# Kernel optimization log

Measured on AMD Instinct MI355X. Metric: run time of the kernel, lower is better.

Reference implementation:

```python
import jax, jax.numpy as jnp
import numpy as np

EPS_BN = 1e-5
EPS_LN = 1e-5
OUT_H, OUT_W = 256, 256


def conv2d(x, w, b, pad):
    y = jax.lax.conv_general_dilated(x, w, (1, 1), [(pad, pad), (pad, pad)],
                                     dimension_numbers=('NCHW', 'OIHW', 'NCHW'))
    return y + b[None, :, None, None]


def leaky(x):
    return jnp.where(x >= 0, x, 0.2 * x)


def bn_eval(x, g, b):
    # fresh BatchNorm2d in eval mode: running_mean=0, running_var=1
    scale = g / jnp.sqrt(1.0 + EPS_BN)
    return x * scale[None, :, None, None] + b[None, :, None, None]


def resize_bilinear(x, oh, ow):
    # align_corners=True bilinear, separable gathers
    n, c, h, w = x.shape
    sy = jnp.arange(oh, dtype=x.dtype) * ((h - 1) / (oh - 1))
    sx = jnp.arange(ow, dtype=x.dtype) * ((w - 1) / (ow - 1))
    y0 = jnp.clip(jnp.floor(sy).astype(jnp.int32), 0, h - 2)
    x0 = jnp.clip(jnp.floor(sx).astype(jnp.int32), 0, w - 2)
    fy = (sy - y0.astype(x.dtype))[None, None, :, None]
    fx = (sx - x0.astype(x.dtype))[None, None, None, :]
    top = x[:, :, y0, :] * (1 - fy) + x[:, :, y0 + 1, :] * fy        # (n,c,oh,w)
    out = top[:, :, :, x0] * (1 - fx) + top[:, :, :, x0 + 1] * fx    # (n,c,oh,ow)
    return out


def layernorm(x, g, b):
    mu = jnp.mean(x, axis=-1, keepdims=True)
    var = jnp.mean((x - mu) ** 2, axis=-1, keepdims=True)
    return (x - mu) * jax.lax.rsqrt(var + EPS_LN) * g + b


def setup_inputs() -> dict:
    key = jax.random.key(0)
    ks = iter(jax.random.split(key, 64))

    def rn(shape, scale=0.05):
        return (jax.random.normal(next(ks), shape, dtype=jnp.float32) * scale)

    inp = {'x': jax.random.normal(next(ks), (8, 64, 128, 128), dtype=jnp.float32)}
    inp.update(
        r_c7a_w=rn((16, 64, 7, 7)), r_c7a_b=jnp.zeros((16,), jnp.float32),
        r_c1_w=rn((16, 16, 1, 1)), r_c1_b=jnp.zeros((16,), jnp.float32),
        r_bn1_g=1.0 + rn((16,), 0.1), r_bn1_b=jnp.zeros((16,), jnp.float32),
        rb_c1_w=rn((16, 16, 3, 3)), rb_c1_b=jnp.zeros((16,), jnp.float32),
        rb_bn1_g=1.0 + rn((16,), 0.1), rb_bn1_b=jnp.zeros((16,), jnp.float32),
        rb_c2_w=rn((16, 16, 3, 3)), rb_c2_b=jnp.zeros((16,), jnp.float32),
        rb_bn2_g=1.0 + rn((16,), 0.1), rb_bn2_b=jnp.zeros((16,), jnp.float32),
        r_c3_w=rn((16, 16, 3, 3)), r_c3_b=jnp.zeros((16,), jnp.float32),
        r_bn2_g=1.0 + rn((16,), 0.1), r_bn2_b=jnp.zeros((16,), jnp.float32),
        r_c7b_w=rn((64, 16, 7, 7)), r_c7b_b=jnp.zeros((64,), jnp.float32),
        a_k_w=rn((1, 64, 1, 1)), a_k_b=jnp.zeros((1,), jnp.float32),
        a_q_w=rn((1, 64, 1, 1)), a_q_b=jnp.zeros((1,), jnp.float32),
        a_v_w=rn((8, 64, 1, 1)), a_v_b=jnp.zeros((8,), jnp.float32),
        a_r_w=rn((64, 8, 1, 1)), a_r_b=jnp.zeros((64,), jnp.float32),
        t_ln_g=jnp.ones((64,), jnp.float32), t_ln_b=jnp.zeros((64,), jnp.float32),
        t_fc1_w=rn((64, 64)), t_fc1_b=jnp.zeros((64,), jnp.float32),
        t_fc2_w=rn((64, 64)), t_fc2_b=jnp.zeros((64,), jnp.float32),
    )
    return inp


def reference(x, r_c7a_w, r_c7a_b, r_c1_w, r_c1_b, r_bn1_g, r_bn1_b,
              rb_c1_w, rb_c1_b, rb_bn1_g, rb_bn1_b, rb_c2_w, rb_c2_b,
              rb_bn2_g, rb_bn2_b, r_c3_w, r_c3_b, r_bn2_g, r_bn2_b,
              r_c7b_w, r_c7b_b, a_k_w, a_k_b, a_q_w, a_q_b, a_v_w, a_v_b,
              a_r_w, a_r_b, t_ln_g, t_ln_b, t_fc1_w, t_fc1_b, t_fc2_w, t_fc2_b):
    # ---- Resizer ----
    identity = resize_bilinear(x, OUT_H, OUT_W)
    y = leaky(conv2d(x, r_c7a_w, r_c7a_b, 3))
    y = bn_eval(leaky(conv2d(y, r_c1_w, r_c1_b, 0)), r_bn1_g, r_bn1_b)
    y = resize_bilinear(y, OUT_H, OUT_W)
    conv_identity = y
    z = leaky(bn_eval(conv2d(y, rb_c1_w, rb_c1_b, 1), rb_bn1_g, rb_bn1_b))
    z = bn_eval(conv2d(z, rb_c2_w, rb_c2_b, 1), rb_bn2_g, rb_bn2_b) + y
    z = bn_eval(conv2d(z, r_c3_w, r_c3_b, 1), r_bn2_g, r_bn2_b) + conv_identity
    out = conv2d(z, r_c7b_w, r_c7b_b, 3) + identity

    # ---- EfficientAttention (key_channels=1, head_count=1, value_channels=8) ----
    n, c, h, w = out.shape
    hw = h * w
    k = conv2d(out, a_k_w, a_k_b, 0).reshape(n, 1, hw)
    q = conv2d(out, a_q_w, a_q_b, 0).reshape(n, 1, hw)
    v = conv2d(out, a_v_w, a_v_b, 0).reshape(n, 8, hw)
    key = jax.nn.softmax(k, axis=2)            # softmax over spatial positions
    query = jax.nn.softmax(q, axis=1)          # size-1 channel axis -> ones (faithful)
    context = jnp.einsum('nkp,nvp->nkv', key, v)          # (n,1,8)
    att = jnp.einsum('nkv,nkp->nvp', context, query)      # (n,8,hw)
    out = conv2d(att.reshape(n, 8, h, w), a_r_w, a_r_b, 0) + out

    # ---- TransformerBlock (identity conv, 1 encoder: x + MLP(LN(x))) ----
    t = out.reshape(n, c, hw).transpose(2, 0, 1)          # (hw, n, c)
    tn = layernorm(t, t_ln_g, t_ln_b)
    m = jax.nn.gelu(tn @ t_fc1_w.T + t_fc1_b, approximate=False) @ t_fc2_w.T + t_fc2_b
    t = t + m
    return t.transpose(1, 2, 0).reshape(n, c, h, w)
```

## Files before the change

kernel.cpp:

```cpp
#include <hip/hip_runtime.h>
#include <math.h>

#define DI __device__ __forceinline__
#define HW128 (128*128)
#define HW256 (256*256)

__device__ const float BN_RS = 0.9999950000374997f;

DI float leakyf(float x){ return x >= 0.f ? x : 0.2f*x; }

DI unsigned short f2bf(float f){
    unsigned u = __float_as_uint(f);
    return (unsigned short)((u + 0x7fffu + ((u >> 16) & 1u)) >> 16);
}
DI void unpack2(unsigned u, float& lo, float& hi){
    lo = __uint_as_float(u << 16);
    hi = __uint_as_float(u & 0xffff0000u);
}
DI void load8(const uint4* s, size_t idx, unsigned* d){
    uint4 t0 = s[idx], t1 = s[idx + 1];
    d[0]=t0.x; d[1]=t0.y; d[2]=t0.z; d[3]=t0.w;
    d[4]=t1.x; d[5]=t1.y; d[6]=t1.z; d[7]=t1.w;
}

typedef __attribute__((ext_vector_type(8))) short short8v;
typedef __attribute__((ext_vector_type(4))) float float4v;

__global__ __launch_bounds__(256) void prepack(
    const float* __restrict__ w7a, const float* __restrict__ w1,
    const float* __restrict__ w3a, const float* __restrict__ b3a, const float* __restrict__ g3a, const float* __restrict__ be3a,
    const float* __restrict__ w3b, const float* __restrict__ b3b, const float* __restrict__ g3b, const float* __restrict__ be3b,
    const float* __restrict__ w3c, const float* __restrict__ b3c, const float* __restrict__ g3c, const float* __restrict__ be3c,
    const float* __restrict__ w7b, const float* __restrict__ fc1w, const float* __restrict__ fc2w,
    unsigned short* __restrict__ p7aB, float* __restrict__ p1,
    float* __restrict__ q3a, float* __restrict__ q3b, float* __restrict__ q3c,
    unsigned short* __restrict__ w3aB, unsigned short* __restrict__ w3bB, unsigned short* __restrict__ w3cB,
    unsigned short* __restrict__ pwB,
    unsigned short* __restrict__ pwT1, unsigned short* __restrict__ pwT2)
{
    int i = blockIdx.x * 256 + threadIdx.x;
    if (i < 57344) {
        int g = i / 14336, rem = i - g*14336;
        int ks = rem >> 9, oc = (rem >> 5) & 15, k = rem & 31;
        int ky = ks >> 2, kx = ((ks & 3) << 1) + (k >> 4), ic = g*16 + (k & 15);
        p7aB[i] = (kx < 7) ? f2bf(w7a[(oc*64 + ic)*49 + ky*7 + kx]) : (unsigned short)0;
    }
    if (i < 57344) {
        int ks = i >> 11, oc = (i >> 5) & 63, k = i & 31;
        int ky = ks >> 2, kx = ((ks & 3) << 1) + (k >> 4), ic = k & 31 & 15;
        ic = k & 15;
        pwB[i] = (kx < 7) ? f2bf(w7b[((oc*16 + ic)*7 + ky)*7 + kx]) : (unsigned short)0;
    }
    if (i < 3072) {
        int ks = i >> 9, oc = (i >> 5) & 15, k = i & 31;
        int ky = ks >> 1, kx = ((ks & 1) << 1) + (k >> 4), ic = k & 15;
        if (kx < 3) {
            int src = (oc*16 + ic)*9 + ky*3 + kx;
            w3aB[i] = f2bf(w3a[src] * (g3a[oc]*BN_RS));
            w3bB[i] = f2bf(w3b[src] * (g3b[oc]*BN_RS));
            w3cB[i] = f2bf(w3c[src] * (g3c[oc]*BN_RS));
        } else {
            w3aB[i] = 0; w3bB[i] = 0; w3cB[i] = 0;
        }
    }
    if (i < 256) { int oc = i & 15, ic = i >> 4; p1[i] = w1[oc*16 + ic]; }
    if (i < 16) {
        q3a[i] = b3a[i]*(g3a[i]*BN_RS) + be3a[i];
        q3b[i] = b3b[i]*(g3b[i]*BN_RS) + be3b[i];
        q3c[i] = b3c[i]*(g3c[i]*BN_RS) + be3c[i];
    }
    if (i < 4096) { pwT1[i] = f2bf(fc1w[i]); pwT2[i] = f2bf(fc2w[i]); }
}

__global__ __launch_bounds__(256) void x_to_ci(
    const float* __restrict__ x, unsigned short* __restrict__ xci)
{
    int idx = blockIdx.x*256 + threadIdx.x;
    int p = idx & 16383, gn = idx >> 14;
    int g = gn & 3, n = gn >> 2;
    const float* xb = x + (size_t)(n*64 + g*16)*HW128 + p;
    unsigned q[8];
#pragma unroll
    for (int h = 0; h < 8; ++h) {
        float a0 = xb[(size_t)(2*h)*HW128];
        float a1 = xb[(size_t)(2*h + 1)*HW128];
        q[h] = (unsigned)f2bf(a0) | ((unsigned)f2bf(a1) << 16);
    }
    uint4* dst = (uint4*)xci + (size_t)idx*2;
    dst[0] = make_uint4(q[0], q[1], q[2], q[3]);
    dst[1] = make_uint4(q[4], q[5], q[6], q[7]);
}

__global__ __launch_bounds__(256) void conv7a_mfma(
    const unsigned short* __restrict__ xci,
    const unsigned short* __restrict__ pw,
    const float* __restrict__ b7a, const float* __restrict__ p1,
    const float* __restrict__ b1, const float* __restrict__ bng,
    const float* __restrict__ bnb, unsigned short* __restrict__ y2ci)
{
    __shared__ __align__(16) unsigned char lds[17408];
    unsigned short* tile = (unsigned short*)lds;
    float* P16 = (float*)lds;

    const int tid = threadIdx.x;
    const int n = blockIdx.z, ox = blockIdx.x*16, oy = blockIdx.y*16;
    const int w = tid >> 6, l = tid & 63, lg = l >> 4, ln = l & 15;

    float4v acc[4];
#pragma unroll
    for (int mi = 0; mi < 4; ++mi) acc[mi] = (float4v){0.f,0.f,0.f,0.f};

    const uint4* xc4 = (const uint4*)xci;
    uint4* tl4 = (uint4*)tile;
    const short8v* Bb = (const short8v*)pw;

    for (int g = 0; g < 4; ++g) {
        __syncthreads();
        for (int u = tid; u < 1056; u += 256) {
            int r = u / 48, s = u - r*48;
            int y = oy + r - 3, xcol = ox + (s >> 1) - 3;
            uint4 v = make_uint4(0u,0u,0u,0u);
            if (y >= 0 && y < 128 && xcol >= 0 && xcol < 128)
                v = xc4[((size_t)(n*4 + g)*16384 + y*128 + xcol)*2 + (s & 1)];
            tl4[u] = v;
        }
        __syncthreads();
        for (int ks = 0; ks < 28; ++ks) {
            const int ky = ks >> 2, kxp = (ks & 3) << 1;
            short8v b = Bb[(g*28 + ks)*64 + ln*4 + lg];
            short8v a[4];
#pragma unroll
            for (int mi = 0; mi < 4; ++mi) {
                int row = (4*w + mi) + ky;
                a[mi] = *(const short8v*)(tile + (row*24 + ln + kxp)*16 + lg*8);
            }
#pragma unroll
            for (int mi = 0; mi < 4; ++mi)
                acc[mi] = __builtin_amdgcn_mfma_f32_16x16x32_bf16(a[mi], b, acc[mi], 0, 0, 0);
        }
    }
    __syncthreads();
    const float bo = b7a[ln];
#pragma unroll
    for (int mi = 0; mi < 4; ++mi)
#pragma unroll
        for (int r = 0; r < 4; ++r)
            P16[((4*w + mi)*16 + lg*4 + r)*17 + ln] = leakyf(acc[mi][r] + bo);
    __syncthreads();
    const int py = tid >> 4, pxx = tid & 15;
    float lv[16];
#pragma unroll
    for (int ic = 0; ic < 16; ++ic) lv[ic] = P16[tid*17 + ic];
    float u16[16];
#pragma unroll
    for (int o = 0; o < 16; ++o) {
        float u = b1[o];
#pragma unroll
        for (int ic = 0; ic < 16; ++ic) u += lv[ic] * p1[ic*16 + o];
        u = leakyf(u);
        u16[o] = u * (bng[o]*BN_RS) + bnb[o];
    }
    const int p = (oy + py)*128 + ox + pxx;
    unsigned q[8];
#pragma unroll
    for (int h = 0; h < 8; ++h)
        q[h] = (unsigned)f2bf(u16[2*h]) | ((unsigned)f2bf(u16[2*h+1]) << 16);
    uint4* dst = (uint4*)y2ci + (size_t)(n*16384 + p)*2;
    dst[0] = make_uint4(q[0], q[1], q[2], q[3]);
    dst[1] = make_uint4(q[4], q[5], q[6], q[7]);
}

__global__ __launch_bounds__(256) void resize_ci(
    const unsigned short* __restrict__ y2ci, unsigned short* __restrict__ yci)
{
    const int n = blockIdx.z;
    const int ox = blockIdx.x*16 + threadIdx.x;
    const int oy = blockIdx.y*16 + threadIdx.y;
    float sy = oy * (127.f/255.f), sx = ox * (127.f/255.f);
    int y0 = min((int)sy, 126), x0 = min((int)sx, 126);
    float fy = sy - y0, fx = sx - x0;
    const uint4* src = (const uint4*)y2ci;
    size_t i00 = ((size_t)n*16384 + y0*128 + x0)*2;
    unsigned A00[8], A01[8], A10[8], A11[8];
    load8(src, i00,       A00);
    load8(src, i00 + 2,   A01);
    load8(src, i00 + 256, A10);
    load8(src, i00 + 258, A11);
    unsigned q[8];
#pragma unroll
    for (int h = 0; h < 8; ++h) {
        float l00, h00, l01, h01, l10, h10, l11, h11;
        unpack2(A00[h], l00, h00); unpack2(A01[h], l01, h01);
        unpack2(A10[h], l10, h10); unpack2(A11[h], l11, h11);
        float lo = (l00*(1.f-fx) + l01*fx)*(1.f-fy) + (l10*(1.f-fx) + l11*fx)*fy;
        float hi = (h00*(1.f-fx) + h01*fx)*(1.f-fy) + (h10*(1.f-fx) + h11*fx)*fy;
        q[h] = (unsigned)f2bf(lo) | ((unsigned)f2bf(hi) << 16);
    }
    uint4* dst = (uint4*)yci + ((size_t)n*65536 + oy*256 + ox)*2;
    dst[0] = make_uint4(q[0], q[1], q[2], q[3]);
    dst[1] = make_uint4(q[4], q[5], q[6], q[7]);
}

template<int MODE>
__global__ __launch_bounds__(256) void conv3_mfma(
    const unsigned short* __restrict__ in_ci,
    const unsigned short* __restrict__ wB, const float* __restrict__ q3,
    const unsigned short* __restrict__ res_ci,
    unsigned short* __restrict__ out_ci)
{
    __shared__ __align__(16) unsigned char lds[17408];
    unsigned short* tile = (unsigned short*)lds;
    float* P16 = (float*)lds;

    const int tid = threadIdx.x;
    const int n = blockIdx.z, ox = blockIdx.x*16, oy = blockIdx.y*16;
    const int w = tid >> 6, l = tid & 63, lg = l >> 4, ln = l & 15;

    const uint4* zc = (const uint4*)in_ci;
    uint4* tl4 = (uint4*)tile;
    for (int u = tid; u < 720; u += 256) {
        int r = u / 40, s = u - r*40;
        int y = oy + r - 1, xcol = ox + (s >> 1) - 1;
        uint4 v = make_uint4(0u,0u,0u,0u);
        if (y >= 0 && y < 256 && xcol >= 0 && xcol < 256)
            v = zc[((size_t)n*65536 + y*256 + xcol)*2 + (s & 1)];
        tl4[u] = v;
    }
    __syncthreads();

    float4v acc[4];
#pragma unroll
    for (int mi = 0; mi < 4; ++mi) acc[mi] = (float4v){0.f,0.f,0.f,0.f};
    const short8v* Bb = (const short8v*)wB;
#pragma unroll
    for (int ks = 0; ks < 6; ++ks) {
        const int ky = ks >> 1, kxp = (ks & 1) << 1;
        short8v b = Bb[(ks*16 + ln)*4 + lg];
        short8v a[4];
#pragma unroll
        for (int mi = 0; mi < 4; ++mi) {
            int row = (4*w + mi) + ky;
            a[mi] = *(const short8v*)(tile + (row*20 + ln + kxp)*16 + lg*8);
        }
#pragma unroll
        for (int mi = 0; mi < 4; ++mi)
            acc[mi] = __builtin_amdgcn_mfma_f32_16x16x32_bf16(a[mi], b, acc[mi], 0, 0, 0);
    }
    __syncthreads();
#pragma unroll
    for (int mi = 0; mi < 4; ++mi)
#pragma unroll
        for (int r = 0; r < 4; ++r)
            P16[((4*w + mi)*16 + lg*4 + r)*17 + ln] = acc[mi][r];
    __syncthreads();

    const int py = tid >> 4, pxx = tid & 15;
    const int p = (oy + py)*256 + ox + pxx;
    float u16[16];
#pragma unroll
    for (int o = 0; o < 16; ++o) u16[o] = P16[tid*17 + o] + q3[o];
    if (MODE == 0) {
#pragma unroll
        for (int o = 0; o < 16; ++o) u16[o] = leakyf(u16[o]);
    } else {
        unsigned R[8];
        load8((const uint4*)res_ci, ((size_t)n*65536 + p)*2, R);
#pragma unroll
        for (int h = 0; h < 8; ++h) {
            float lo, hi; unpack2(R[h], lo, hi);
            u16[2*h] += lo; u16[2*h+1] += hi;
        }
    }
    unsigned q[8];
#pragma unroll
    for (int h = 0; h < 8; ++h)
        q[h] = (unsigned)f2bf(u16[2*h]) | ((unsigned)f2bf(u16[2*h+1]) << 16);
    uint4* dst = (uint4*)out_ci + ((size_t)n*65536 + p)*2;
    dst[0] = make_uint4(q[0], q[1], q[2], q[3]);
    dst[1] = make_uint4(q[4], q[5], q[6], q[7]);
}

__global__ __launch_bounds__(256) void conv7b_mfma(
    const unsigned short* __restrict__ z_ci,
    const unsigned short* __restrict__ pwB,
    const float* __restrict__ x,
    const float* __restrict__ bias,
    const float* __restrict__ akw, const float* __restrict__ akb,
    float* __restrict__ out0, float* __restrict__ kbuf)
{
    __shared__ __align__(16) unsigned char lds[17408 + 12800];
    unsigned short* tile = (unsigned short*)lds;
    float* P16 = (float*)lds;
    unsigned short* xt16 = (unsigned short*)(lds + 17408);

    const int tid = threadIdx.x;
    const int n = blockIdx.z, ox = blockIdx.x*16, oy = blockIdx.y*16;
    const float SC = 127.f/255.f;
    const int ybase = (int)(oy*SC), xbase = (int)(ox*SC);

    const uint4* zc = (const uint4*)z_ci;
    uint4* tl4 = (uint4*)tile;
    for (int u = tid; u < 1056; u += 256) {
        int r = u / 48, s = u - r*48;
        int y = oy + r - 3, xcol = ox + (s >> 1) - 3;
        uint4 v = make_uint4(0u, 0u, 0u, 0u);
        if (y >= 0 && y < 256 && xcol >= 0 && xcol < 256)
            v = zc[(size_t)((n*256 + y)*256 + xcol)*2 + (s & 1)];
        tl4[u] = v;
    }
    for (int u = tid; u < 6400; u += 256) {
        int ch = u / 100, rem = u - ch*100;
        int r = rem / 10, c = rem - r*10;
        int y = ybase + r, xc = xbase + c;
        float v = 0.f;
        if (y < 128 && xc < 128) v = x[(size_t)(n*64 + ch)*HW128 + y*128 + xc];
        xt16[(r*10 + c)*64 + ch] = f2bf(v);
    }
    __syncthreads();

    const int w = tid >> 6, l = tid & 63;
    const int lg = l >> 4, ln = l & 15;
    float4v acc[4][4];
#pragma unroll
    for (int mi = 0; mi < 4; ++mi)
#pragma unroll
        for (int nt = 0; nt < 4; ++nt)
            acc[mi][nt] = (float4v){0.f, 0.f, 0.f, 0.f};

    const short8v* Bb = (const short8v*)pwB;
    for (int ks = 0; ks < 28; ++ks) {
        const int ky = ks >> 2, kxp = (ks & 3) << 1;
        short8v a[4], b[4];
#pragma unroll
        for (int mi = 0; mi < 4; ++mi) {
            int row = (4*w + mi) + ky;
            a[mi] = *(const short8v*)(tile + (row*24 + ln + kxp)*16 + lg*8);
        }
#pragma unroll
        for (int nt = 0; nt < 4; ++nt)
            b[nt] = Bb[ks*256 + nt*64 + ln*4 + lg];
#pragma unroll
        for (int mi = 0; mi < 4; ++mi)
#pragma unroll
            for (int nt = 0; nt < 4; ++nt)
                acc[mi][nt] = __builtin_amdgcn_mfma_f32_16x16x32_bf16(
                    a[mi], b[nt], acc[mi][nt], 0, 0, 0);
    }

    const int py = tid >> 4, pxx = tid & 15;
    const int ohy = oy + py, ohx = ox + pxx;
    float sy = ohy*SC, sx = ohx*SC;
    int y0 = min((int)sy, 126), x0 = min((int)sx, 126);
    float fy = sy - y0, fx = sx - x0;
    const int ly = y0 - ybase, lx = x0 - xbase;
    const int p = ohy*256 + ohx;
    const uint4* xt4 = (const uint4*)xt16;
    const size_t q00 = ((size_t)(ly*10 + lx)*64) >> 3;
    float kacc = akb[0];

    for (int nt = 0; nt < 4; ++nt) {
        __syncthreads();
#pragma unroll
        for (int mi = 0; mi < 4; ++mi)
#pragma unroll
            for (int r = 0; r < 4; ++r)
                P16[((4*w + mi)*16 + lg*4 + r)*17 + ln] = acc[mi][nt][r];
        __syncthreads();
        unsigned A00[8], A01[8], A10[8], A11[8];
        size_t qb = q00 + nt*2;
        load8(xt4, qb,      A00);
        load8(xt4, qb + 8,  A01);
        load8(xt4, qb + 80, A10);
        load8(xt4, qb + 88, A11);
        float u16[16];
#pragma unroll
        for (int h = 0; h < 8; ++h) {
            float l00, h00, l01, h01, l10, h10, l11, h11;
            unpack2(A00[h], l00, h00); unpack2(A01[h], l01, h01);
            unpack2(A10[h], l10, h10); unpack2(A11[h], l11, h11);
            u16[2*h]   = (l00*(1.f-fx) + l01*fx)*(1.f-fy) + (l10*(1.f-fx) + l11*fx)*fy;
            u16[2*h+1] = (h00*(1.f-fx) + h01*fx)*(1.f-fy) + (h10*(1.f-fx) + h11*fx)*fy;
        }
#pragma unroll
        for (int o = 0; o < 16; ++o) {
            int oc = nt*16 + o;
            float u = P16[tid*17 + o] + bias[oc] + u16[o];
            out0[(size_t)(n*64 + oc)*HW256 + p] = u;
            kacc += akw[oc] * u;
        }
    }
    kbuf[n*65536 + p] = kacc;
}

__global__ __launch_bounds__(1024) void softmax_stats(
    const float* __restrict__ kb, float* __restrict__ st)
{
    __shared__ float red[16];
    __shared__ float bc;
    const int n = blockIdx.x, tid = threadIdx.x;
    const float* kp = kb + n*65536;
    float mx = -3.0e38f;
    for (int i = tid; i < 65536; i += 1024) mx = fmaxf(mx, kp[i]);
#pragma unroll
    for (int off = 1; off < 64; off <<= 1) mx = fmaxf(mx, __shfl_xor(mx, off));
    int w = tid >> 6, l = tid & 63;
    if (l == 0) red[w] = mx;
    __syncthreads();
    if (tid == 0) {
        float m = red[0];
        for (int i = 1; i < 16; ++i) m = fmaxf(m, red[i]);
        bc = m;
    }
    __syncthreads();
    float MX = bc;
    float s = 0.f;
    for (int i = tid; i < 65536; i += 1024) s += __expf(kp[i] - MX);
#pragma unroll
    for (int off = 1; off < 64; off <<= 1) s += __shfl_xor(s, off);
    __syncthreads();
    if (l == 0) red[w] = s;
    __syncthreads();
    if (tid == 0) {
        float S = 0.f;
        for (int i = 0; i < 16; ++i) S += red[i];
        st[n] = MX; st[8 + n] = 1.f / S;
    }
}

__global__ __launch_bounds__(256) void att_wsum(
    const float* __restrict__ out0, const float* __restrict__ kb,
    const float* __restrict__ st, float* __restrict__ Sp)
{
    const int cg = blockIdx.x, pc = blockIdx.y, n = blockIdx.z, c0 = cg*8;
    const float mx = st[n];
    const float* kp = kb + n*65536 + pc*16384;
    const float* base = out0 + (size_t)(n*64 + c0)*HW256 + pc*16384;
    float acc[8];
#pragma unroll
    for (int c = 0; c < 8; ++c) acc[c] = 0.f;
    for (int p = threadIdx.x; p < 16384; p += 256) {
        float e = __expf(kp[p] - mx);
#pragma unroll
        for (int c = 0; c < 8; ++c) acc[c] += e * base[c*HW256 + p];
    }
#pragma unroll
    for (int c = 0; c < 8; ++c)
#pragma unroll
        for (int off = 1; off < 64; off <<= 1) acc[c] += __shfl_xor(acc[c], off);
    __shared__ float red[4][8];
    int w = threadIdx.x >> 6, l = threadIdx.x & 63;
    if (l == 0) {
#pragma unroll
        for (int c = 0; c < 8; ++c) red[w][c] = acc[c];
    }
    __syncthreads();
    if (threadIdx.x < 8)
        Sp[n*256 + pc*64 + c0 + threadIdx.x] =
            red[0][threadIdx.x] + red[1][threadIdx.x] + red[2][threadIdx.x] + red[3][threadIdx.x];
}

__global__ __launch_bounds__(512) void ctx_addc(
    const float* __restrict__ Sp, const float* __restrict__ st,
    const float* __restrict__ avw, const float* __restrict__ avb,
    const float* __restrict__ arw, const float* __restrict__ arb,
    float* __restrict__ addc)
{
    __shared__ float ctx[8][8];
    const int tid = threadIdx.x;
    if (tid < 64) {
        int n = tid >> 3, vc = tid & 7;
        float s = 0.f;
        for (int c = 0; c < 64; ++c) {
            float Sv = Sp[n*256 + c] + Sp[n*256 + 64 + c]
                     + Sp[n*256 + 128 + c] + Sp[n*256 + 192 + c];
            s += avw[vc*64 + c] * Sv;
        }
        ctx[n][vc] = s * st[8 + n] + avb[vc];
    }
    __syncthreads();
    int n = tid >> 6, c = tid & 63;
    float a = arb[c];
#pragma unroll
    for (int vc = 0; vc < 8; ++vc) a += arw[c*8 + vc] * ctx[n][vc];
    addc[n*64 + c] = a;
}

__global__ __launch_bounds__(256) void transformer_mfma(
    float* __restrict__ out0, const float* __restrict__ addc,
    const float* __restrict__ lng, const float* __restrict__ lnb,
    const unsigned short* __restrict__ W1b, const float* __restrict__ fc1b,
    const unsigned short* __restrict__ W2b, const float* __restrict__ fc2b)
{
    __shared__ __align__(16) unsigned char lds[34816 + 18432];
    float*          Xt = (float*)lds;
    unsigned short* Xb = (unsigned short*)(lds + 34816);
    unsigned short* Hb = Xb;

    const int tid = threadIdx.x;
    const int n = blockIdx.x >> 9;
    const int p0 = (blockIdx.x & 511) << 7;
    const float* ac = addc + n*64;

#pragma unroll
    for (int k = 0; k < 8; ++k) {
        int v = k*256 + tid;
        int c = v >> 5, i4 = (v & 31) << 2;
        float4v q = *(const float4v*)(out0 + (size_t)(n*64 + c)*HW256 + p0 + i4);
        float a = ac[c];
#pragma unroll
        for (int r = 0; r < 4; ++r) q[r] += a;
        *(float4v*)&Xt[c*136 + i4] = q;
    }
    __syncthreads();

    if (tid < 128) {
        float t[64];
#pragma unroll
        for (int c = 0; c < 64; ++c) t[c] = Xt[c*136 + tid];
        float mu = 0.f;
#pragma unroll
        for (int c = 0; c < 64; ++c) mu += t[c];
        mu *= (1.f/64.f);
        float var = 0.f;
#pragma unroll
        for (int c = 0; c < 64; ++c) { float d = t[c] - mu; var += d*d; }
        var *= (1.f/64.f);
        float rs = rsqrtf(var + 1e-5f);
#pragma unroll
        for (int c8 = 0; c8 < 8; ++c8) {
            short8v pk;
#pragma unroll
            for (int e = 0; e < 8; ++e) {
                int c = c8*8 + e;
                pk[e] = (short)f2bf((t[c] - mu)*rs*lng[c] + lnb[c]);
            }
            *(short8v*)&Xb[tid*72 + c8*8] = pk;
        }
    }
    __syncthreads();

    const int w = tid >> 6, l = tid & 63, lg = l >> 4, ln = l & 15;

    float4v acc1[2][4];
#pragma unroll
    for (int mt = 0; mt < 2; ++mt)
#pragma unroll
        for (int nt = 0; nt < 4; ++nt) acc1[mt][nt] = (float4v){0.f,0.f,0.f,0.f};
#pragma unroll
    for (int kk = 0; kk < 2; ++kk) {
        short8v a[2], b[4];
#pragma unroll
        for (int mt = 0; mt < 2; ++mt)
            a[mt] = *(const short8v*)&Xb[(w*32 + mt*16 + ln)*72 + kk*32 + lg*8];
#pragma unroll
        for (int nt = 0; nt < 4; ++nt)
            b[nt] = *(const short8v*)&W1b[(nt*16 + ln)*64 + kk*32 + lg*8];
#pragma unroll
        for (int mt = 0; mt < 2; ++mt)
#pragma unroll
            for (int nt = 0; nt < 4; ++nt)
                acc1[mt][nt] = __builtin_amdgcn_mfma_f32_16x16x32_bf16(
                    a[mt], b[nt], acc1[mt][nt], 0, 0, 0);
    }
    __syncthreads();
#pragma unroll
    for (int mt = 0; mt < 2; ++mt)
#pragma unroll
        for (int nt = 0; nt < 4; ++nt) {
            int j = nt*16 + ln;
            float bj = fc1b[j];
#pragma unroll
            for (int r = 0; r < 4; ++r) {
                int token = w*32 + mt*16 + lg*4 + r;
                float m = acc1[mt][nt][r] + bj;
                float g = 0.5f*m*(1.f + erff(m*0.70710678118654752f));
                Hb[token*72 + j] = f2bf(g);
            }
        }
    __syncthreads();

    float4v acc2[2][4];
#pragma unroll
    for (int mt = 0; mt < 2; ++mt)
#pragma unroll
        for (int nt = 0; nt < 4; ++nt) acc2[mt][nt] = (float4v){0.f,0.f,0.f,0.f};
#pragma unroll
    for (int kk = 0; kk < 2; ++kk) {
        short8v a[2], b[4];
#pragma unroll
        for (int mt = 0; mt < 2; ++mt)
            a[mt] = *(const short8v*)&Hb[(w*32 + mt*16 + ln)*72 + kk*32 + lg*8];
#pragma unroll
        for (int nt = 0; nt < 4; ++nt)
            b[nt] = *(const short8v*)&W2b[(nt*16 + ln)*64 + kk*32 + lg*8];
#pragma unroll
        for (int mt = 0; mt < 2; ++mt)
#pragma unroll
            for (int nt = 0; nt < 4; ++nt)
                acc2[mt][nt] = __builtin_amdgcn_mfma_f32_16x16x32_bf16(
                    a[mt], b[nt], acc2[mt][nt], 0, 0, 0);
    }
#pragma unroll
    for (int mt = 0; mt < 2; ++mt)
#pragma unroll
        for (int nt = 0; nt < 4; ++nt) {
            int c = nt*16 + ln;
            int tb = w*32 + mt*16 + lg*4;
            float add = fc2b[c];
            float4v t4 = *(const float4v*)&Xt[c*136 + tb];
            float* dst = out0 + (size_t)(n*64 + c)*HW256 + p0 + tb;
            float4v o;
#pragma unroll
            for (int r = 0; r < 4; ++r) o[r] = t4[r] + acc2[mt][nt][r] + add;
            *(float4v*)dst = o;
        }
}

extern "C" void kernel_launch(void* const* d_in, const int* in_sizes, int n_in,
                              void* d_out, int out_size, void* d_ws, size_t ws_size,
                              hipStream_t stream)
{
    (void)in_sizes; (void)n_in; (void)out_size; (void)ws_size;
    const float* x    = (const float*)d_in[0];
    const float* w7a  = (const float*)d_in[1];
    const float* b7a  = (const float*)d_in[2];
    const float* w1   = (const float*)d_in[3];
    const float* b1   = (const float*)d_in[4];
    const float* g1   = (const float*)d_in[5];
    const float* be1  = (const float*)d_in[6];
    const float* w3a  = (const float*)d_in[7];
    const float* b3a  = (const float*)d_in[8];
    const float* g3a  = (const float*)d_in[9];
    const float* be3a = (const float*)d_in[10];
    const float* w3b  = (const float*)d_in[11];
    const float* b3b  = (const float*)d_in[12];
    const float* g3b  = (const float*)d_in[13];
    const float* be3b = (const float*)d_in[14];
    const float* w3c  = (const float*)d_in[15];
    const float* b3c  = (const float*)d_in[16];
    const float* g3c  = (const float*)d_in[17];
    const float* be3c = (const float*)d_in[18];
    const float* w7b  = (const float*)d_in[19];
    const float* b7b  = (const float*)d_in[20];
    const float* akw  = (const float*)d_in[21];
    const float* akb  = (const float*)d_in[22];
    const float* avw  = (const float*)d_in[25];
    const float* avb  = (const float*)d_in[26];
    const float* arw  = (const float*)d_in[27];
    const float* arb  = (const float*)d_in[28];
    const float* lng  = (const float*)d_in[29];
    const float* lnb  = (const float*)d_in[30];
    const float* fc1w = (const float*)d_in[31];
    const float* fc1b = (const float*)d_in[32];
    const float* fc2w = (const float*)d_in[33];
    const float* fc2b = (const float*)d_in[34];

    float* ws = (float*)d_ws;
    unsigned short* y2ci = (unsigned short*)ws;
    unsigned short* yci  = (unsigned short*)(ws + 1048576);
    unsigned short* z1ci = (unsigned short*)(ws + 1048576 + 4194304);
    unsigned short* z2ci = (unsigned short*)(ws + 1048576 + 2*4194304);
    unsigned short* xci  = (unsigned short*)(ws + 1048576 + 3*4194304);
    float* o_k  = ws + 1048576 + 4*4194304;
    float* o_st = o_k + 524288;
    float* o_Sp = o_st + 64;
    float* o_ad = o_Sp + 2048;
    unsigned short* p7aB = (unsigned short*)(o_ad + 512);
    float* p1   = o_ad + 512 + 28672;
    float* q3a  = p1 + 256;
    float* q3b  = q3a + 16;
    float* q3c  = q3b + 16;
    unsigned short* w3aB = (unsigned short*)(q3c + 16);
    unsigned short* w3bB = w3aB + 3072;
    unsigned short* w3cB = w3bB + 3072;
    unsigned short* pwB  = w3cB + 3072;
    unsigned short* pwT1 = pwB + 57344;
    unsigned short* pwT2 = pwT1 + 4096;

    unsigned short* z3ci = z1ci;
    float* out0 = (float*)d_out;

    prepack<<<224, 256, 0, stream>>>(w7a, w1, w3a,b3a,g3a,be3a, w3b,b3b,g3b,be3b,
                                     w3c,b3c,g3c,be3c, w7b, fc1w, fc2w,
                                     p7aB, p1, q3a, q3b, q3c, w3aB, w3bB, w3cB,
                                     pwB, pwT1, pwT2);
    x_to_ci<<<2048, 256, 0, stream>>>(x, xci);
    conv7a_mfma<<<dim3(8,8,8), 256, 0, stream>>>(xci, p7aB, b7a, p1, b1, g1, be1, y2ci);
    resize_ci<<<dim3(16,16,8), dim3(16,16), 0, stream>>>(y2ci, yci);
    conv3_mfma<0><<<dim3(16,16,8), 256, 0, stream>>>(yci,  w3aB, q3a, nullptr, z1ci);
    conv3_mfma<1><<<dim3(16,16,8), 256, 0, stream>>>(z1ci, w3bB, q3b, yci,     z2ci);
    conv3_mfma<1><<<dim3(16,16,8), 256, 0, stream>>>(z2ci, w3cB, q3c, yci,     z3ci);
    conv7b_mfma<<<dim3(16,16,8), 256, 0, stream>>>(z3ci, pwB, x, b7b, akw, akb, out0, o_k);
    softmax_stats<<<8, 1024, 0, stream>>>(o_k, o_st);
    att_wsum<<<dim3(8,4,8), 256, 0, stream>>>(out0, o_k, o_st, o_Sp);
    ctx_addc<<<1, 512, 0, stream>>>(o_Sp, o_st, avw, avb, arw, arb, o_ad);
    transformer_mfma<<<4096, 256, 0, stream>>>(out0, o_ad, lng, lnb, pwT1, fc1b, pwT2, fc2b);
}
```

Baseline: 370.2 us.

## Load residual x tile from bf16 channel-interleaved buffer and split softmax stats

```diff
diff --git a/kernel.cpp b/kernel.cpp
--- a/kernel.cpp
+++ b/kernel.cpp
@@ -47,8 +47,7 @@
     }
     if (i < 57344) {
         int ks = i >> 11, oc = (i >> 5) & 63, k = i & 31;
-        int ky = ks >> 2, kx = ((ks & 3) << 1) + (k >> 4), ic = k & 31 & 15;
-        ic = k & 15;
+        int ky = ks >> 2, kx = ((ks & 3) << 1) + (k >> 4), ic = k & 15;
         pwB[i] = (kx < 7) ? f2bf(w7b[((oc*16 + ic)*7 + ky)*7 + kx]) : (unsigned short)0;
     }
     if (i < 3072) {
@@ -283,12 +282,12 @@
 __global__ __launch_bounds__(256) void conv7b_mfma(
     const unsigned short* __restrict__ z_ci,
     const unsigned short* __restrict__ pwB,
-    const float* __restrict__ x,
+    const unsigned short* __restrict__ xci,
     const float* __restrict__ bias,
     const float* __restrict__ akw, const float* __restrict__ akb,
     float* __restrict__ out0, float* __restrict__ kbuf)
 {
-    __shared__ __align__(16) unsigned char lds[17408 + 12800];
+    __shared__ __align__(16) unsigned char lds[17408 + 14400];
     unsigned short* tile = (unsigned short*)lds;
     float* P16 = (float*)lds;
     unsigned short* xt16 = (unsigned short*)(lds + 17408);
@@ -308,13 +307,19 @@
             v = zc[(size_t)((n*256 + y)*256 + xcol)*2 + (s & 1)];
         tl4[u] = v;
     }
-    for (int u = tid; u < 6400; u += 256) {
-        int ch = u / 100, rem = u - ch*100;
-        int r = rem / 10, c = rem - r*10;
-        int y = ybase + r, xc = xbase + c;
-        float v = 0.f;
-        if (y < 128 && xc < 128) v = x[(size_t)(n*64 + ch)*HW128 + y*128 + xc];
-        xt16[(r*10 + c)*64 + ch] = f2bf(v);
+    const uint4* xc4 = (const uint4*)xci;
+    uint4* xt4 = (uint4*)xt16;
+    for (int u = tid; u < 900; u += 256) {
+        int p = u / 9, s = u - p*9;
+        uint4 v = make_uint4(0u, 0u, 0u, 0u);
+        if (s < 8) {
+            int g = s >> 1, half = s & 1;
+            int r = p / 10, c = p - r*10;
+            int y = ybase + r, xcc = xbase + c;
+            if (y < 128 && xcc < 128)
+                v = xc4[((size_t)(n*4 + g)*16384 + y*128 + xcc)*2 + half];
+        }
+        xt4[u] = v;
     }
     __syncthreads();
 
@@ -354,8 +359,8 @@
     float fy = sy - y0, fx = sx - x0;
     const int ly = y0 - ybase, lx = x0 - xbase;
     const int p = ohy*256 + ohx;
-    const uint4* xt4 = (const uint4*)xt16;
-    const size_t q00 = ((size_t)(ly*10 + lx)*64) >> 3;
+    const uint4* xt4c = (const uint4*)xt16;
+    const size_t q00 = (size_t)(ly*10 + lx)*9;
     float kacc = akb[0];
 
     for (int nt = 0; nt < 4; ++nt) {
@@ -368,10 +373,10 @@
         __syncthreads();
         unsigned A00[8], A01[8], A10[8], A11[8];
         size_t qb = q00 + nt*2;
-        load8(xt4, qb,      A00);
-        load8(xt4, qb + 8,  A01);
-        load8(xt4, qb + 80, A10);
-        load8(xt4, qb + 88, A11);
+        load8(xt4c, qb,      A00);
+        load8(xt4c, qb + 9,  A01);
+        load8(xt4c, qb + 90, A10);
+        load8(xt4c, qb + 99, A11);
         float u16[16];
 #pragma unroll
         for (int h = 0; h < 8; ++h) {
@@ -392,37 +397,47 @@
     kbuf[n*65536 + p] = kacc;
 }
 
-__global__ __launch_bounds__(1024) void softmax_stats(
-    const float* __restrict__ kb, float* __restrict__ st)
-{
-    __shared__ float red[16];
-    __shared__ float bc;
-    const int n = blockIdx.x, tid = threadIdx.x;
-    const float* kp = kb + n*65536;
+__global__ __launch_bounds__(256) void softmax_part(
+    const float* __restrict__ kb, float* __restrict__ pst)
+{
+    __shared__ float red[4];
+    __shared__ float bcast;
+    const int pc = blockIdx.x, n = blockIdx.y, tid = threadIdx.x;
+    const float* kp = kb + n*65536 + pc*8192;
     float mx = -3.0e38f;
-    for (int i = tid; i < 65536; i += 1024) mx = fmaxf(mx, kp[i]);
+    for (int i = tid; i < 8192; i += 256) mx = fmaxf(mx, kp[i]);
 #pragma unroll
     for (int off = 1; off < 64; off <<= 1) mx = fmaxf(mx, __shfl_xor(mx, off));
     int w = tid >> 6, l = tid & 63;
     if (l == 0) red[w] = mx;
     __syncthreads();
+    if (tid == 0) bcast = fmaxf(fmaxf(red[0], red[1]), fmaxf(red[2], red[3]));
+    __syncthreads();
+    float BM = bcast;
+    float s = 0.f;
+    for (int i = tid; i < 8192; i += 256) s += __expf(kp[i] - BM);
+#pragma unroll
+    for (int off = 1; off < 64; off <<= 1) s += __shfl_xor(s, off);
+    __syncthreads();
+    if (l == 0) red[w] = s;
+    __syncthreads();
     if (tid == 0) {
-        float m = red[0];
-        for (int i = 1; i < 16; ++i) m = fmaxf(m, red[i]);
-        bc = m;
-    }
-    __syncthreads();
-    float MX = bc;
-    float s = 0.f;
-    for (int i = tid; i < 65536; i += 1024) s += __expf(kp[i] - MX);
-#pragma unroll
-    for (int off = 1; off < 64; off <<= 1) s += __shfl_xor(s, off);
-    __syncthreads();
-    if (l == 0) red[w] = s;
-    __syncthreads();
-    if (tid == 0) {
+        pst[(n*8 + pc)*2]     = BM;
+        pst[(n*8 + pc)*2 + 1] = red[0] + red[1] + red[2] + red[3];
+    }
+}
+
+__global__ __launch_bounds__(64) void softmax_comb(
+    const float* __restrict__ pst, float* __restrict__ st)
+{
+    int tid = threadIdx.x;
+    if (tid < 8) {
+        int n = tid;
+        float MX = -3.0e38f;
+        for (int c = 0; c < 8; ++c) MX = fmaxf(MX, pst[(n*8 + c)*2]);
         float S = 0.f;
-        for (int i = 0; i < 16; ++i) S += red[i];
+        for (int c = 0; c < 8; ++c)
+            S += pst[(n*8 + c)*2 + 1] * __expf(pst[(n*8 + c)*2] - MX);
         st[n] = MX; st[8 + n] = 1.f / S;
     }
 }
@@ -661,10 +676,11 @@
     unsigned short* z1ci = (unsigned short*)(ws + 1048576 + 4194304);
     unsigned short* z2ci = (unsigned short*)(ws + 1048576 + 2*4194304);
     unsigned short* xci  = (unsigned short*)(ws + 1048576 + 3*4194304);
-    float* o_k  = ws + 1048576 + 4*4194304;
-    float* o_st = o_k + 524288;
-    float* o_Sp = o_st + 64;
-    float* o_ad = o_Sp + 2048;
+    float* o_k   = ws + 1048576 + 4*4194304;
+    float* o_st  = o_k + 524288;
+    float* o_pst = o_st + 64;
+    float* o_Sp  = o_pst + 128;
+    float* o_ad  = o_Sp + 2048;
     unsigned short* p7aB = (unsigned short*)(o_ad + 512);
     float* p1   = o_ad + 512 + 28672;
     float* q3a  = p1 + 256;
@@ -690,8 +706,9 @@
     conv3_mfma<0><<<dim3(16,16,8), 256, 0, stream>>>(yci,  w3aB, q3a, nullptr, z1ci);
     conv3_mfma<1><<<dim3(16,16,8), 256, 0, stream>>>(z1ci, w3bB, q3b, yci,     z2ci);
     conv3_mfma<1><<<dim3(16,16,8), 256, 0, stream>>>(z2ci, w3cB, q3c, yci,     z3ci);
-    conv7b_mfma<<<dim3(16,16,8), 256, 0, stream>>>(z3ci, pwB, x, b7b, akw, akb, out0, o_k);
-    softmax_stats<<<8, 1024, 0, stream>>>(o_k, o_st);
+    conv7b_mfma<<<dim3(16,16,8), 256, 0, stream>>>(z3ci, pwB, xci, b7b, akw, akb, out0, o_k);
+    softmax_part<<<dim3(8,8), 256, 0, stream>>>(o_k, o_pst);
+    softmax_comb<<<1, 64, 0, stream>>>(o_pst, o_st);
     att_wsum<<<dim3(8,4,8), 256, 0, stream>>>(out0, o_k, o_st, o_Sp);
     ctx_addc<<<1, 512, 0, stream>>>(o_Sp, o_st, avw, avb, arw, arb, o_ad);
     transformer_mfma<<<4096, 256, 0, stream>>>(out0, o_ad, lng, lnb, pwT1, fc1b, pwT2, fc2b);
```

Result: faster. 324.2 us (-12.4%).
